# Performance work log

Hardware: AMD Instinct MI355X
Metric: run time of the kernel (lower is better)

## Reference

```python
import jax, jax.numpy as jnp
import numpy as np

B, S, E, H = 4, 2048, 1024, 16
D = E // H
N_INF = -10000.0


def setup_inputs() -> dict:
    key = jax.random.key(0)
    ks = jax.random.split(key, 12)
    sc = 1.0 / np.sqrt(E)
    inp = {
        "q": jax.random.normal(ks[0], (B, S, E), jnp.float32),
        "k": jax.random.normal(ks[1], (B, S, E), jnp.float32),
        "v": jax.random.normal(ks[2], (B, S, E), jnp.float32),
        "mask": jax.random.randint(ks[3], (1, 1, S, S), 0, 2, jnp.int32),
        "wq": jax.random.normal(ks[4], (E, E), jnp.float32) * sc,
        "bq": jax.random.normal(ks[5], (E,), jnp.float32) * sc,
        "wk": jax.random.normal(ks[6], (E, E), jnp.float32) * sc,
        "bk": jax.random.normal(ks[7], (E,), jnp.float32) * sc,
        "wv": jax.random.normal(ks[8], (E, E), jnp.float32) * sc,
        "bv": jax.random.normal(ks[9], (E,), jnp.float32) * sc,
        "wo": jax.random.normal(ks[10], (E, E), jnp.float32) * sc,
        "bo": jax.random.normal(ks[11], (E,), jnp.float32) * sc,
    }
    return inp


def _split(x):
    # [B,S,E] -> [B,H,S,D]
    return x.reshape(B, S, H, D).transpose(0, 2, 1, 3)


def reference(q, k, v, mask, wq, bq, wk, bk, wv, bv, wo, bo):
    # Linear projections (torch Linear: x @ W^T + b)
    qh = _split(q @ wq.T + bq)
    kh = _split(k @ wk.T + bk)
    vh = _split(v @ wv.T + bv)
    # scaled dot-product attention
    scores = jnp.einsum("bhqd,bhkd->bhqk", qh, kh) / jnp.sqrt(jnp.float32(D))
    scores = jnp.where(mask == 0, jnp.float32(N_INF), scores)
    attn = jax.nn.softmax(scores, axis=-1)
    out = jnp.einsum("bhqk,bhkd->bhqd", attn, vh)
    # concat heads: [B,H,S,D] -> [B,S,E]
    out = out.transpose(0, 2, 1, 3).reshape(B, S, E)
    return out @ wo.T + bo
```

## Files before the change

kernel.cpp:

```cpp
#include <hip/hip_runtime.h>

typedef __attribute__((ext_vector_type(8))) short short8;
typedef __attribute__((ext_vector_type(4))) float f32x4;
typedef __attribute__((ext_vector_type(4))) int int4v;
typedef __attribute__((ext_vector_type(2))) unsigned int uint2v;
typedef __attribute__((ext_vector_type(4))) unsigned int uint4v;
typedef __attribute__((ext_vector_type(4))) unsigned short u16x4;

#define MFMA16x16x32(a, b, c) __builtin_amdgcn_mfma_f32_16x16x32_bf16((a), (b), (c), 0, 0, 0)

#define QK_SCALE 0.18033688011112042f
#define MASKB_BF16 ((unsigned short)0xC2C0)

__device__ __forceinline__ unsigned short f2bf(float f) {
  unsigned u = __builtin_bit_cast(unsigned, f);
  u += 0x7fffu + ((u >> 16) & 1u);
  return (unsigned short)(u >> 16);
}

__device__ __forceinline__ float bf2f(unsigned short s) {
  return __builtin_bit_cast(float, (unsigned)s << 16);
}

__device__ __forceinline__ unsigned cvt_pk(float lo, float hi) {
  unsigned r;
  asm("v_cvt_pk_bf16_f32 %0, %1, %2" : "=v"(r) : "v"(lo), "v"(hi));
  return r;
}

__global__ __launch_bounds__(256) void prep_bf16(const float* __restrict__ in,
                                                 unsigned short* __restrict__ out) {
  const int i = (blockIdx.x * 256 + threadIdx.x) * 8;
  f32x4 a = *(const f32x4*)(in + i);
  f32x4 b = *(const f32x4*)(in + i + 4);
  uint4v r;
  r[0] = cvt_pk(a[0], a[1]);
  r[1] = cvt_pk(a[2], a[3]);
  r[2] = cvt_pk(b[0], b[1]);
  r[3] = cvt_pk(b[2], b[3]);
  *(uint4v*)(out + i) = r;
}

__global__ __launch_bounds__(256) void prep_bias(const int* __restrict__ mask,
                                                 unsigned short* __restrict__ bias) {
  const int i = (blockIdx.x * 256 + threadIdx.x) * 8;
  int4v m0 = *(const int4v*)(mask + i);
  int4v m1 = *(const int4v*)(mask + i + 4);
  short8 s;
#pragma unroll
  for (int j = 0; j < 4; ++j) s[j] = (m0[j] == 0) ? (short)MASKB_BF16 : (short)0;
#pragma unroll
  for (int j = 0; j < 4; ++j) s[4 + j] = (m1[j] == 0) ? (short)MASKB_BF16 : (short)0;
  *(short8*)(bias + i) = s;
}

template <int EPI>
__global__ __launch_bounds__(256) void gemm_bt(
    const unsigned short* __restrict__ A, const unsigned short* __restrict__ B,
    const float* __restrict__ bias, void* __restrict__ out,
    int M, int N, int K) {
  __shared__ unsigned short Asm[128][72];
  __shared__ unsigned short Bsm[128][72];
  const int tid = threadIdx.x;
  const int lane = tid & 63;
  const int wid = tid >> 6;
  const int wr = wid >> 1, wc = wid & 1;
  const int mbase = blockIdx.y * 128, nbase = blockIdx.x * 128;

  f32x4 acc[4][4] = {};

  for (int k0 = 0; k0 < K; k0 += 64) {
#pragma unroll
    for (int r = 0; r < 4; ++r) {
      const int c = tid + 256 * r;
      const int row = c >> 3, col = (c & 7) << 3;
      *(short8*)&Asm[row][col] = *(const short8*)(A + (size_t)(mbase + row) * K + k0 + col);
      *(short8*)&Bsm[row][col] = *(const short8*)(B + (size_t)(nbase + row) * K + k0 + col);
    }
    __syncthreads();
#pragma unroll
    for (int ks = 0; ks < 2; ++ks) {
      const int kk = ks * 32 + (lane >> 4) * 8;
      short8 af[4], bfv[4];
#pragma unroll
      for (int t = 0; t < 4; ++t) {
        af[t] = *(const short8*)&Asm[wr * 64 + t * 16 + (lane & 15)][kk];
        bfv[t] = *(const short8*)&Bsm[wc * 64 + t * 16 + (lane & 15)][kk];
      }
#pragma unroll
      for (int tm = 0; tm < 4; ++tm)
#pragma unroll
        for (int tn = 0; tn < 4; ++tn)
          acc[tm][tn] = MFMA16x16x32(af[tm], bfv[tn], acc[tm][tn]);
    }
    __syncthreads();
  }

  float bn[4];
  if (EPI == 0 || EPI == 2) {
#pragma unroll
    for (int tn = 0; tn < 4; ++tn)
      bn[tn] = bias[nbase + wc * 64 + tn * 16 + (lane & 15)];
  }
  float bm[4][4];
  if (EPI == 1) {
#pragma unroll
    for (int tm = 0; tm < 4; ++tm)
#pragma unroll
      for (int i = 0; i < 4; ++i)
        bm[tm][i] = bias[mbase + wr * 64 + tm * 16 + (lane >> 4) * 4 + i];
  }
#pragma unroll
  for (int tm = 0; tm < 4; ++tm) {
#pragma unroll
    for (int i = 0; i < 4; ++i) {
      const int m = mbase + wr * 64 + tm * 16 + (lane >> 4) * 4 + i;
#pragma unroll
      for (int tn = 0; tn < 4; ++tn) {
        const int n = nbase + wc * 64 + tn * 16 + (lane & 15);
        const float v = acc[tm][tn][i] + (EPI == 1 ? bm[tm][i] : bn[tn]);
        if (EPI == 0) {
          const size_t idx =
              (((size_t)(m >> 11) * 16 + (n >> 6)) * 2048 + (m & 2047)) * 64 + (n & 63);
          ((unsigned short*)out)[idx] = f2bf(v);
        } else if (EPI == 1) {
          const size_t idx =
              (((size_t)(n >> 11) * 16 + (m >> 6)) * 64 + (m & 63)) * 2048 + (n & 2047);
          ((unsigned short*)out)[idx] = f2bf(v);
        } else {
          ((float*)out)[(size_t)m * N + n] = v;
        }
      }
    }
  }
}

__global__ __launch_bounds__(256) void attn_fused(
    const unsigned short* __restrict__ Qh, const unsigned short* __restrict__ Kh,
    const unsigned short* __restrict__ VT, const unsigned short* __restrict__ Bias,
    unsigned short* __restrict__ Ob) {
  __shared__ unsigned short Kl[64][72];
  __shared__ unsigned short Vl[64][72];
  __shared__ unsigned short Pl[128][72];
  const int tid = threadIdx.x, lane = tid & 63, w = tid >> 6;
  const int qt = blockIdx.x & 15, bh = blockIdx.x >> 4;
  const int q0 = qt << 7;
  const unsigned short* Qb = Qh + (size_t)bh * (2048 * 64);
  const unsigned short* Kb = Kh + (size_t)bh * (2048 * 64);
  const unsigned short* Vb = VT + (size_t)bh * (64 * 2048);

  short8 qf[2][2];
#pragma unroll
  for (int ks = 0; ks < 2; ++ks)
#pragma unroll
    for (int tq = 0; tq < 2; ++tq)
      qf[ks][tq] = *(const short8*)(Qb +
          (size_t)(q0 + w * 32 + tq * 16 + (lane & 15)) * 64 + ks * 32 + (lane >> 4) * 8);

  const unsigned short* brow[2];
#pragma unroll
  for (int tq = 0; tq < 2; ++tq)
    brow[tq] = Bias + (size_t)(q0 + w * 32 + tq * 16 + (lane & 15)) * 2048 + ((lane >> 4) << 2);

  u16x4 bcur[2][4];
#pragma unroll
  for (int tq = 0; tq < 2; ++tq)
#pragma unroll
    for (int tkv = 0; tkv < 4; ++tkv) bcur[tq][tkv] = *(const u16x4*)(brow[tq] + tkv * 16);

  f32x4 acc[2][4] = {};
  float l_run[2] = {0.f, 0.f};

  for (int kt = 0; kt < 32; ++kt) {
    const int kv0 = kt << 6;
    __syncthreads();
#pragma unroll
    for (int r = 0; r < 2; ++r) {
      const int c = tid + 256 * r;
      const int row = c >> 3, col = (c & 7) << 3;
      *(short8*)&Kl[row][col] = *(const short8*)(Kb + (size_t)(kv0 + row) * 64 + col);
      *(short8*)&Vl[row][col] = *(const short8*)(Vb + (size_t)row * 2048 + kv0 + col);
    }
    u16x4 bnxt[2][4];
    {
      const int kvn = (kt < 31) ? kv0 + 64 : 0;
#pragma unroll
      for (int tq = 0; tq < 2; ++tq)
#pragma unroll
        for (int tkv = 0; tkv < 4; ++tkv)
          bnxt[tq][tkv] = *(const u16x4*)(brow[tq] + kvn + tkv * 16);
    }
    __syncthreads();

    f32x4 st[4][2] = {};
    __builtin_amdgcn_s_setprio(1);
#pragma unroll
    for (int ks = 0; ks < 2; ++ks) {
      const int kk = ks * 32 + (lane >> 4) * 8;
      short8 kf[4];
#pragma unroll
      for (int t = 0; t < 4; ++t) kf[t] = *(const short8*)&Kl[t * 16 + (lane & 15)][kk];
#pragma unroll
      for (int tkv = 0; tkv < 4; ++tkv)
#pragma unroll
        for (int tq = 0; tq < 2; ++tq)
          st[tkv][tq] = MFMA16x16x32(kf[tkv], qf[ks][tq], st[tkv][tq]);
    }
    __builtin_amdgcn_s_setprio(0);

#pragma unroll
    for (int tq = 0; tq < 2; ++tq) {
      float rsum = 0.f;
#pragma unroll
      for (int tkv = 0; tkv < 4; ++tkv) {
        const float x0 =
            __builtin_amdgcn_exp2f(__builtin_fmaf(st[tkv][tq][0], QK_SCALE, bf2f(bcur[tq][tkv][0])));
        const float x1 =
            __builtin_amdgcn_exp2f(__builtin_fmaf(st[tkv][tq][1], QK_SCALE, bf2f(bcur[tq][tkv][1])));
        const float x2 =
            __builtin_amdgcn_exp2f(__builtin_fmaf(st[tkv][tq][2], QK_SCALE, bf2f(bcur[tq][tkv][2])));
        const float x3 =
            __builtin_amdgcn_exp2f(__builtin_fmaf(st[tkv][tq][3], QK_SCALE, bf2f(bcur[tq][tkv][3])));
        rsum += (x0 + x1) + (x2 + x3);
        uint2v pk;
        pk[0] = cvt_pk(x0, x1);
        pk[1] = cvt_pk(x2, x3);
        *(uint2v*)&Pl[w * 32 + tq * 16 + (lane & 15)][tkv * 16 + ((lane >> 4) << 2)] = pk;
      }
      l_run[tq] += rsum;
    }

    __builtin_amdgcn_s_setprio(1);
#pragma unroll
    for (int ks = 0; ks < 2; ++ks) {
      const int kk = ks * 32 + (lane >> 4) * 8;
      short8 pa[2], vf[4];
#pragma unroll
      for (int t = 0; t < 2; ++t)
        pa[t] = *(const short8*)&Pl[w * 32 + t * 16 + (lane & 15)][kk];
#pragma unroll
      for (int t = 0; t < 4; ++t) vf[t] = *(const short8*)&Vl[t * 16 + (lane & 15)][kk];
#pragma unroll
      for (int tm = 0; tm < 2; ++tm)
#pragma unroll
        for (int tn = 0; tn < 4; ++tn)
          acc[tm][tn] = MFMA16x16x32(pa[tm], vf[tn], acc[tm][tn]);
    }
    __builtin_amdgcn_s_setprio(0);

#pragma unroll
    for (int tq = 0; tq < 2; ++tq)
#pragma unroll
      for (int tkv = 0; tkv < 4; ++tkv) bcur[tq][tkv] = bnxt[tq][tkv];
  }

#pragma unroll
  for (int tm = 0; tm < 2; ++tm) {
    l_run[tm] += __shfl_xor(l_run[tm], 16);
    l_run[tm] += __shfl_xor(l_run[tm], 32);
  }

  const int b = bh >> 4, h = bh & 15;
#pragma unroll
  for (int tm = 0; tm < 2; ++tm) {
#pragma unroll
    for (int i = 0; i < 4; ++i) {
      const float lv = __shfl(l_run[tm], ((lane >> 4) << 2) + i);
      const float rl = 1.0f / lv;
      const int q = q0 + w * 32 + tm * 16 + ((lane >> 4) << 2) + i;
      unsigned short* orow = Ob + ((size_t)b * 2048 + q) * 1024 + h * 64;
#pragma unroll
      for (int tn = 0; tn < 4; ++tn)
        orow[tn * 16 + (lane & 15)] = f2bf(acc[tm][tn][i] * rl);
    }
  }
}

extern "C" void kernel_launch(void* const* d_in, const int* in_sizes, int n_in,
                              void* d_out, int out_size, void* d_ws, size_t ws_size,
                              hipStream_t stream) {
  const float* q = (const float*)d_in[0];
  const float* k = (const float*)d_in[1];
  const float* v = (const float*)d_in[2];
  const int* mask = (const int*)d_in[3];
  const float* wq = (const float*)d_in[4];
  const float* bq = (const float*)d_in[5];
  const float* wk = (const float*)d_in[6];
  const float* bk = (const float*)d_in[7];
  const float* wv = (const float*)d_in[8];
  const float* bv = (const float*)d_in[9];
  const float* wo = (const float*)d_in[10];
  const float* bo = (const float*)d_in[11];

  char* ws = (char*)d_ws;
  unsigned short* Qh = (unsigned short*)ws;
  unsigned short* Kh = (unsigned short*)(ws + (16u << 20));
  unsigned short* VT = (unsigned short*)(ws + (32u << 20));
  unsigned short* Bias = (unsigned short*)(ws + (48u << 20));
  unsigned short* S = (unsigned short*)(ws + (56u << 20));
  unsigned short* Ob = S;
  unsigned short* wqb = (unsigned short*)(ws + (72u << 20));
  unsigned short* wkb = wqb + (1u << 20);
  unsigned short* wvb = wqb + (2u << 20);
  unsigned short* wob = wqb + (3u << 20);

  const dim3 blk(256);
  prep_bf16<<<dim3(512), blk, 0, stream>>>(wq, wqb);
  prep_bf16<<<dim3(512), blk, 0, stream>>>(wk, wkb);
  prep_bf16<<<dim3(512), blk, 0, stream>>>(wv, wvb);
  prep_bf16<<<dim3(512), blk, 0, stream>>>(wo, wob);
  prep_bias<<<dim3(2048), blk, 0, stream>>>(mask, Bias);

  prep_bf16<<<dim3(4096), blk, 0, stream>>>(q, S);
  gemm_bt<0><<<dim3(8, 64), blk, 0, stream>>>(S, wqb, bq, (void*)Qh, 8192, 1024, 1024);
  prep_bf16<<<dim3(4096), blk, 0, stream>>>(k, S);
  gemm_bt<0><<<dim3(8, 64), blk, 0, stream>>>(S, wkb, bk, (void*)Kh, 8192, 1024, 1024);
  prep_bf16<<<dim3(4096), blk, 0, stream>>>(v, S);
  gemm_bt<1><<<dim3(64, 8), blk, 0, stream>>>(wvb, S, bv, (void*)VT, 1024, 8192, 1024);
  attn_fused<<<dim3(1024), blk, 0, stream>>>(Qh, Kh, VT, Bias, Ob);
  gemm_bt<2><<<dim3(8, 64), blk, 0, stream>>>(Ob, wob, bo, d_out, 8192, 1024, 1024);
}
```

Measured before the change: 291.6 us.

## Keep P in registers, fold scale and mask bias into QK MFMA accumulators

The attention kernel drops the LDS round-trip for P by feeding the exp'd probabilities straight from registers into 16x16x16 bf16 MFMAs. The QK scale moves into the Q projection epilogue, and the mask bias becomes an fp32 tensor loaded as the initial accumulator, which removes the per-element FMA and bf16 decode. It also remaps blocks across the grid for L2 locality, adds a waves-per-EU launch bound, and reuses workspace regions for the weights. The fp32 bias doubles mask-read bandwidth and the narrower MFMAs issue more instructions.

```diff
diff --git a/kernel.cpp b/kernel.cpp
--- a/kernel.cpp
+++ b/kernel.cpp
@@ -1,16 +1,15 @@
 #include <hip/hip_runtime.h>
 
 typedef __attribute__((ext_vector_type(8))) short short8;
+typedef __attribute__((ext_vector_type(4))) short s16x4;
 typedef __attribute__((ext_vector_type(4))) float f32x4;
 typedef __attribute__((ext_vector_type(4))) int int4v;
 typedef __attribute__((ext_vector_type(2))) unsigned int uint2v;
 typedef __attribute__((ext_vector_type(4))) unsigned int uint4v;
-typedef __attribute__((ext_vector_type(4))) unsigned short u16x4;
 
 #define MFMA16x16x32(a, b, c) __builtin_amdgcn_mfma_f32_16x16x32_bf16((a), (b), (c), 0, 0, 0)
 
 #define QK_SCALE 0.18033688011112042f
-#define MASKB_BF16 ((unsigned short)0xC2C0)
 
 __device__ __forceinline__ unsigned short f2bf(float f) {
   unsigned u = __builtin_bit_cast(unsigned, f);
@@ -18,14 +17,16 @@
   return (unsigned short)(u >> 16);
 }
 
-__device__ __forceinline__ float bf2f(unsigned short s) {
-  return __builtin_bit_cast(float, (unsigned)s << 16);
-}
-
 __device__ __forceinline__ unsigned cvt_pk(float lo, float hi) {
   unsigned r;
   asm("v_cvt_pk_bf16_f32 %0, %1, %2" : "=v"(r) : "v"(lo), "v"(hi));
   return r;
+}
+
+__device__ __forceinline__ f32x4 mfma16(s16x4 a, s16x4 b, f32x4 c) {
+  f32x4 d;
+  asm("v_mfma_f32_16x16x16_bf16 %0, %1, %2, %3" : "=v"(d) : "v"(a), "v"(b), "v"(c));
+  return d;
 }
 
 __global__ __launch_bounds__(256) void prep_bf16(const float* __restrict__ in,
@@ -41,24 +42,25 @@
   *(uint4v*)(out + i) = r;
 }
 
-__global__ __launch_bounds__(256) void prep_bias(const int* __restrict__ mask,
-                                                 unsigned short* __restrict__ bias) {
+__global__ __launch_bounds__(256) void prep_biasf(const int* __restrict__ mask,
+                                                  float* __restrict__ bias) {
   const int i = (blockIdx.x * 256 + threadIdx.x) * 8;
   int4v m0 = *(const int4v*)(mask + i);
   int4v m1 = *(const int4v*)(mask + i + 4);
-  short8 s;
-#pragma unroll
-  for (int j = 0; j < 4; ++j) s[j] = (m0[j] == 0) ? (short)MASKB_BF16 : (short)0;
-#pragma unroll
-  for (int j = 0; j < 4; ++j) s[4 + j] = (m1[j] == 0) ? (short)MASKB_BF16 : (short)0;
-  *(short8*)(bias + i) = s;
+  f32x4 o0, o1;
+#pragma unroll
+  for (int j = 0; j < 4; ++j) o0[j] = (m0[j] == 0) ? -96.0f : 0.0f;
+#pragma unroll
+  for (int j = 0; j < 4; ++j) o1[j] = (m1[j] == 0) ? -96.0f : 0.0f;
+  *(f32x4*)(bias + i) = o0;
+  *(f32x4*)(bias + i + 4) = o1;
 }
 
 template <int EPI>
 __global__ __launch_bounds__(256) void gemm_bt(
     const unsigned short* __restrict__ A, const unsigned short* __restrict__ B,
     const float* __restrict__ bias, void* __restrict__ out,
-    int M, int N, int K) {
+    int M, int N, int K, float scl) {
   __shared__ unsigned short Asm[128][72];
   __shared__ unsigned short Bsm[128][72];
   const int tid = threadIdx.x;
@@ -118,7 +120,7 @@
 #pragma unroll
       for (int tn = 0; tn < 4; ++tn) {
         const int n = nbase + wc * 64 + tn * 16 + (lane & 15);
-        const float v = acc[tm][tn][i] + (EPI == 1 ? bm[tm][i] : bn[tn]);
+        const float v = (acc[tm][tn][i] + (EPI == 1 ? bm[tm][i] : bn[tn])) * scl;
         if (EPI == 0) {
           const size_t idx =
               (((size_t)(m >> 11) * 16 + (n >> 6)) * 2048 + (m & 2047)) * 64 + (n & 63);
@@ -135,15 +137,16 @@
   }
 }
 
-__global__ __launch_bounds__(256) void attn_fused(
+__global__ __launch_bounds__(256, 4) void attn_fused(
     const unsigned short* __restrict__ Qh, const unsigned short* __restrict__ Kh,
-    const unsigned short* __restrict__ VT, const unsigned short* __restrict__ Bias,
+    const unsigned short* __restrict__ VT, const float* __restrict__ Biasf,
     unsigned short* __restrict__ Ob) {
   __shared__ unsigned short Kl[64][72];
   __shared__ unsigned short Vl[64][72];
-  __shared__ unsigned short Pl[128][72];
   const int tid = threadIdx.x, lane = tid & 63, w = tid >> 6;
-  const int qt = blockIdx.x & 15, bh = blockIdx.x >> 4;
+  const int m = lane & 15, g = lane >> 4;
+  const int wg = ((blockIdx.x & 7) << 7) + (blockIdx.x >> 3);
+  const int qt = wg & 15, bh = wg >> 4;
   const int q0 = qt << 7;
   const unsigned short* Qb = Qh + (size_t)bh * (2048 * 64);
   const unsigned short* Kb = Kh + (size_t)bh * (2048 * 64);
@@ -155,18 +158,12 @@
 #pragma unroll
     for (int tq = 0; tq < 2; ++tq)
       qf[ks][tq] = *(const short8*)(Qb +
-          (size_t)(q0 + w * 32 + tq * 16 + (lane & 15)) * 64 + ks * 32 + (lane >> 4) * 8);
-
-  const unsigned short* brow[2];
+          (size_t)(q0 + w * 32 + tq * 16 + m) * 64 + ks * 32 + g * 8);
+
+  const float* brow[2];
 #pragma unroll
   for (int tq = 0; tq < 2; ++tq)
-    brow[tq] = Bias + (size_t)(q0 + w * 32 + tq * 16 + (lane & 15)) * 2048 + ((lane >> 4) << 2);
-
-  u16x4 bcur[2][4];
-#pragma unroll
-  for (int tq = 0; tq < 2; ++tq)
-#pragma unroll
-    for (int tkv = 0; tkv < 4; ++tkv) bcur[tq][tkv] = *(const u16x4*)(brow[tq] + tkv * 16);
+    brow[tq] = Biasf + (size_t)(q0 + w * 32 + tq * 16 + m) * 2048 + g * 4;
 
   f32x4 acc[2][4] = {};
   float l_run[2] = {0.f, 0.f};
@@ -181,25 +178,26 @@
       *(short8*)&Kl[row][col] = *(const short8*)(Kb + (size_t)(kv0 + row) * 64 + col);
       *(short8*)&Vl[row][col] = *(const short8*)(Vb + (size_t)row * 2048 + kv0 + col);
     }
-    u16x4 bnxt[2][4];
-    {
-      const int kvn = (kt < 31) ? kv0 + 64 : 0;
-#pragma unroll
-      for (int tq = 0; tq < 2; ++tq)
-#pragma unroll
-        for (int tkv = 0; tkv < 4; ++tkv)
-          bnxt[tq][tkv] = *(const u16x4*)(brow[tq] + kvn + tkv * 16);
-    }
+    f32x4 bini[2][4];
+#pragma unroll
+    for (int tq = 0; tq < 2; ++tq)
+#pragma unroll
+      for (int tkv = 0; tkv < 4; ++tkv)
+        bini[tq][tkv] = *(const f32x4*)(brow[tq] + kv0 + tkv * 16);
     __syncthreads();
 
-    f32x4 st[4][2] = {};
+    f32x4 st[4][2];
+#pragma unroll
+    for (int tkv = 0; tkv < 4; ++tkv)
+#pragma unroll
+      for (int tq = 0; tq < 2; ++tq) st[tkv][tq] = bini[tq][tkv];
     __builtin_amdgcn_s_setprio(1);
 #pragma unroll
     for (int ks = 0; ks < 2; ++ks) {
-      const int kk = ks * 32 + (lane >> 4) * 8;
+      const int kk = ks * 32 + g * 8;
       short8 kf[4];
 #pragma unroll
-      for (int t = 0; t < 4; ++t) kf[t] = *(const short8*)&Kl[t * 16 + (lane & 15)][kk];
+      for (int t = 0; t < 4; ++t) kf[t] = *(const short8*)&Kl[t * 16 + m][kk];
 #pragma unroll
       for (int tkv = 0; tkv < 4; ++tkv)
 #pragma unroll
@@ -208,51 +206,41 @@
     }
     __builtin_amdgcn_s_setprio(0);
 
+    uint2v pa[2][4];
 #pragma unroll
     for (int tq = 0; tq < 2; ++tq) {
-      float rsum = 0.f;
+      float rsum = l_run[tq];
 #pragma unroll
       for (int tkv = 0; tkv < 4; ++tkv) {
-        const float x0 =
-            __builtin_amdgcn_exp2f(__builtin_fmaf(st[tkv][tq][0], QK_SCALE, bf2f(bcur[tq][tkv][0])));
-        const float x1 =
-            __builtin_amdgcn_exp2f(__builtin_fmaf(st[tkv][tq][1], QK_SCALE, bf2f(bcur[tq][tkv][1])));
-        const float x2 =
-            __builtin_amdgcn_exp2f(__builtin_fmaf(st[tkv][tq][2], QK_SCALE, bf2f(bcur[tq][tkv][2])));
-        const float x3 =
-            __builtin_amdgcn_exp2f(__builtin_fmaf(st[tkv][tq][3], QK_SCALE, bf2f(bcur[tq][tkv][3])));
+        const float x0 = __builtin_amdgcn_exp2f(st[tkv][tq][0]);
+        const float x1 = __builtin_amdgcn_exp2f(st[tkv][tq][1]);
+        const float x2 = __builtin_amdgcn_exp2f(st[tkv][tq][2]);
+        const float x3 = __builtin_amdgcn_exp2f(st[tkv][tq][3]);
         rsum += (x0 + x1) + (x2 + x3);
-        uint2v pk;
-        pk[0] = cvt_pk(x0, x1);
-        pk[1] = cvt_pk(x2, x3);
-        *(uint2v*)&Pl[w * 32 + tq * 16 + (lane & 15)][tkv * 16 + ((lane >> 4) << 2)] = pk;
+        pa[tq][tkv][0] = cvt_pk(x0, x1);
+        pa[tq][tkv][1] = cvt_pk(x2, x3);
       }
-      l_run[tq] += rsum;
-    }
-
+      l_run[tq] = rsum;
+    }
+
+    asm volatile("s_nop 1");
     __builtin_amdgcn_s_setprio(1);
 #pragma unroll
-    for (int ks = 0; ks < 2; ++ks) {
-      const int kk = ks * 32 + (lane >> 4) * 8;
-      short8 pa[2], vf[4];
-#pragma unroll
-      for (int t = 0; t < 2; ++t)
-        pa[t] = *(const short8*)&Pl[w * 32 + t * 16 + (lane & 15)][kk];
-#pragma unroll
-      for (int t = 0; t < 4; ++t) vf[t] = *(const short8*)&Vl[t * 16 + (lane & 15)][kk];
+    for (int tn = 0; tn < 4; ++tn) {
+      s16x4 vf[4];
+#pragma unroll
+      for (int tkv = 0; tkv < 4; ++tkv)
+        vf[tkv] = *(const s16x4*)&Vl[tn * 16 + m][tkv * 16 + g * 4];
 #pragma unroll
       for (int tm = 0; tm < 2; ++tm)
 #pragma unroll
-        for (int tn = 0; tn < 4; ++tn)
-          acc[tm][tn] = MFMA16x16x32(pa[tm], vf[tn], acc[tm][tn]);
+        for (int tkv = 0; tkv < 4; ++tkv)
+          acc[tm][tn] = mfma16(__builtin_bit_cast(s16x4, pa[tm][tkv]), vf[tkv], acc[tm][tn]);
     }
     __builtin_amdgcn_s_setprio(0);
-
-#pragma unroll
-    for (int tq = 0; tq < 2; ++tq)
-#pragma unroll
-      for (int tkv = 0; tkv < 4; ++tkv) bcur[tq][tkv] = bnxt[tq][tkv];
-  }
+  }
+
+  asm volatile("s_nop 7\ns_nop 7");
 
 #pragma unroll
   for (int tm = 0; tm < 2; ++tm) {
@@ -265,13 +253,13 @@
   for (int tm = 0; tm < 2; ++tm) {
 #pragma unroll
     for (int i = 0; i < 4; ++i) {
-      const float lv = __shfl(l_run[tm], ((lane >> 4) << 2) + i);
+      const float lv = __shfl(l_run[tm], (g << 2) + i);
       const float rl = 1.0f / lv;
-      const int q = q0 + w * 32 + tm * 16 + ((lane >> 4) << 2) + i;
+      const int q = q0 + w * 32 + tm * 16 + (g << 2) + i;
       unsigned short* orow = Ob + ((size_t)b * 2048 + q) * 1024 + h * 64;
 #pragma unroll
       for (int tn = 0; tn < 4; ++tn)
-        orow[tn * 16 + (lane & 15)] = f2bf(acc[tm][tn][i] * rl);
+        orow[tn * 16 + m] = f2bf(acc[tm][tn][i] * rl);
     }
   }
 }
@@ -296,27 +284,26 @@
   unsigned short* Qh = (unsigned short*)ws;
   unsigned short* Kh = (unsigned short*)(ws + (16u << 20));
   unsigned short* VT = (unsigned short*)(ws + (32u << 20));
-  unsigned short* Bias = (unsigned short*)(ws + (48u << 20));
-  unsigned short* S = (unsigned short*)(ws + (56u << 20));
+  float* Biasf = (float*)(ws + (48u << 20));
+  unsigned short* S = (unsigned short*)(ws + (64u << 20));
   unsigned short* Ob = S;
-  unsigned short* wqb = (unsigned short*)(ws + (72u << 20));
-  unsigned short* wkb = wqb + (1u << 20);
-  unsigned short* wvb = wqb + (2u << 20);
-  unsigned short* wob = wqb + (3u << 20);
+  unsigned short* wqb = Kh;
+  unsigned short* wkb = VT;
+  unsigned short* wvb = (unsigned short*)Biasf;
+  unsigned short* wob = Qh;
 
   const dim3 blk(256);
+  prep_bf16<<<dim3(4096), blk, 0, stream>>>(q, S);
   prep_bf16<<<dim3(512), blk, 0, stream>>>(wq, wqb);
+  gemm_bt<0><<<dim3(8, 64), blk, 0, stream>>>(S, wqb, bq, (void*)Qh, 8192, 1024, 1024, QK_SCALE);
+  prep_bf16<<<dim3(4096), blk, 0, stream>>>(k, S);
   prep_bf16<<<dim3(512), blk, 0, stream>>>(wk, wkb);
+  gemm_bt<0><<<dim3(8, 64), blk, 0, stream>>>(S, wkb, bk, (void*)Kh, 8192, 1024, 1024, 1.0f);
+  prep_bf16<<<dim3(4096), blk, 0, stream>>>(v, S);
   prep_bf16<<<dim3(512), blk, 0, stream>>>(wv, wvb);
+  gemm_bt<1><<<dim3(64, 8), blk, 0, stream>>>(wvb, S, bv, (void*)VT, 1024, 8192, 1024, 1.0f);
+  prep_biasf<<<dim3(2048), blk, 0, stream>>>(mask, Biasf);
+  attn_fused<<<dim3(1024), blk, 0, stream>>>(Qh, Kh, VT, Biasf, Ob);
   prep_bf16<<<dim3(512), blk, 0, stream>>>(wo, wob);
-  prep_bias<<<dim3(2048), blk, 0, stream>>>(mask, Bias);
-
-  prep_bf16<<<dim3(4096), blk, 0, stream>>>(q, S);
-  gemm_bt<0><<<dim3(8, 64), blk, 0, stream>>>(S, wqb, bq, (void*)Qh, 8192, 1024, 1024);
-  prep_bf16<<<dim3(4096), blk, 0, stream>>>(k, S);
-  gemm_bt<0><<<dim3(8, 64), blk, 0, stream>>>(S, wkb, bk, (void*)Kh, 8192, 1024, 1024);
-  prep_bf16<<<dim3(4096), blk, 0, stream>>>(v, S);
-  gemm_bt<1><<<dim3(64, 8), blk, 0, stream>>>(wvb, S, bv, (void*)VT, 1024, 8192, 1024);
-  attn_fused<<<dim3(1024), blk, 0, stream>>>(Qh, Kh, VT, Bias, Ob);
-  gemm_bt<2><<<dim3(8, 64), blk, 0, stream>>>(Ob, wob, bo, d_out, 8192, 1024, 1024);
-}
+  gemm_bt<2><<<dim3(8, 64), blk, 0, stream>>>(Ob, wob, bo, d_out, 8192, 1024, 1024, 1.0f);
+}
```

New measurement: 301.2 us. 1.03x slower.
